# Optimization experiments

Hardware: AMD Instinct MI355X
Metric: run time of the kernel (lower is better)

## Reference

```python
import jax, jax.numpy as jnp
import numpy as np
from jax import lax

USER_NUM = 60000
ITEM_NUM = 40000
N_NODES = USER_NUM + ITEM_NUM
EMB = 64
NNZ = 3200000
N_LAYERS = 3
ALPHA = 0.1


def setup_inputs() -> dict:
    key = jax.random.key(0)
    k1, k2, k3, k4, k5 = jax.random.split(key, 5)
    rows = jax.random.randint(k1, (NNZ,), 0, N_NODES, dtype=jnp.int32)
    cols = jax.random.randint(k2, (NNZ,), 0, N_NODES, dtype=jnp.int32)
    # normalized adjacency values are small positives
    vals = jax.random.uniform(k3, (NNZ,), dtype=jnp.float32) * 0.05
    user_emb = jax.random.normal(k4, (USER_NUM, EMB), dtype=jnp.float32) * 0.1
    item_emb = jax.random.normal(k5, (ITEM_NUM, EMB), dtype=jnp.float32) * 0.1
    return {"rows": rows, "cols": cols, "vals": vals,
            "user_emb": user_emb, "item_emb": item_emb}


def reference(rows, cols, vals, user_emb, item_emb):
    # ego = cat(user, item); e_out starts at zeros (first forward call).
    ego = jnp.concatenate([user_emb, item_emb], axis=0)  # [N, d]
    e0 = jnp.zeros_like(ego)

    def step(e, _):
        # torch.sparse.mm(A, e.clone().detach()) -> SpMM with stop_gradient,
        # matching the original's detach of the propagated state.
        gathered = vals[:, None] * lax.stop_gradient(e)[cols]  # [nnz, d]
        msg = jax.ops.segment_sum(gathered, rows, num_segments=N_NODES)
        e_new = (1.0 - ALPHA) * msg + ego
        return e_new, None

    e_out, _ = lax.scan(step, e0, None, length=N_LAYERS)
    return e_out[:USER_NUM], e_out[USER_NUM:]
```

## Files before the change

kernel.cpp:

```cpp
#include <hip/hip_runtime.h>
#include <hip/hip_fp16.h>


#define USER_NUM 60000
#define ITEM_NUM 40000
#define N_NODES  100000
#define EMB      64
#define NNZ      3200000
#define OMA      0.9f
#define BR       128
#define NB       782
#define TILE     4096
#define CAPB     4480

typedef float f32x4 __attribute__((ext_vector_type(4)));

__global__ __launch_bounds__(256) void conv_init(const float* __restrict__ ue,
                                                 const float* __restrict__ ie,
                                                 __half* __restrict__ dst,
                                                 int* __restrict__ bcursor) {
    int t = blockIdx.x * 256 + threadIdx.x;
    if (t < NB) bcursor[t] = t * CAPB;
    const int total8 = N_NODES * EMB / 8;
    if (t >= total8) return;
    size_t f0 = (size_t)t * 8;
    const size_t usz = (size_t)USER_NUM * EMB;
    const float4* s4 = (f0 < usz) ? (const float4*)(ue + f0)
                                  : (const float4*)(ie + (f0 - usz));
    float4 x = s4[0], y = s4[1];
    union { float4 f4; __half2 h2[4]; } o;
    o.h2[0] = __floats2half2_rn(x.x, x.y);
    o.h2[1] = __floats2half2_rn(x.z, x.w);
    o.h2[2] = __floats2half2_rn(y.x, y.y);
    o.h2[3] = __floats2half2_rn(y.z, y.w);
    ((float4*)dst)[t] = o.f4;
}

__global__ __launch_bounds__(256) void bucket_scatter(const int* __restrict__ rows,
                                                      const int* __restrict__ cols,
                                                      const float* __restrict__ vals,
                                                      int* __restrict__ bcursor,
                                                      int2* __restrict__ ebuf) {
    __shared__ int bins[NB + 1];
    __shared__ int lcur[NB];
    __shared__ int wsum[4];
    __shared__ int2 stage[TILE];
    int t = threadIdx.x;
    int lane = t & 63, w = t >> 6;
    for (int b = t; b <= NB; b += 256) bins[b] = 0;
    __syncthreads();

    int e0 = blockIdx.x * TILE;
    int mybk[16], mypk[16];
    float myv[16];
#pragma unroll
    for (int j = 0; j < 16; ++j) {
        int i = e0 + t + 256 * j;
        mybk[j] = -1;
        if (i < NNZ) {
            int r = rows[i], c = cols[i];
            myv[j]  = vals[i] * OMA;
            mybk[j] = r >> 7;
            mypk[j] = c | ((r & 127) << 17);
            atomicAdd(&bins[mybk[j]], 1);
        }
    }
    __syncthreads();

    int b0 = t * 4;
    int r0 = (b0     < NB) ? bins[b0]     : 0;
    int r1 = (b0 + 1 < NB) ? bins[b0 + 1] : 0;
    int r2 = (b0 + 2 < NB) ? bins[b0 + 2] : 0;
    int r3 = (b0 + 3 < NB) ? bins[b0 + 3] : 0;
    int s = r0 + r1 + r2 + r3;
    int incl = s;
#pragma unroll
    for (int off = 1; off < 64; off <<= 1) {
        int v = __shfl_up(incl, off, 64);
        if (lane >= off) incl += v;
    }
    if (lane == 63) wsum[w] = incl;
    __syncthreads();
    int prefix = 0;
#pragma unroll
    for (int i = 0; i < 4; ++i) if (i < w) prefix += wsum[i];
    int excl = prefix + incl - s;
    if (b0     < NB) { bins[b0]     = excl; lcur[b0]     = excl; excl += r0; }
    if (b0 + 1 < NB) { bins[b0 + 1] = excl; lcur[b0 + 1] = excl; excl += r1; }
    if (b0 + 2 < NB) { bins[b0 + 2] = excl; lcur[b0 + 2] = excl; excl += r2; }
    if (b0 + 3 < NB) { bins[b0 + 3] = excl; lcur[b0 + 3] = excl; excl += r3; }
    if (t == 255) bins[NB] = prefix + incl;
    __syncthreads();

#pragma unroll
    for (int j = 0; j < 16; ++j) {
        if (mybk[j] >= 0) {
            int p = atomicAdd(&lcur[mybk[j]], 1);
            stage[p] = make_int2(mypk[j], __float_as_int(myv[j]));
        }
    }
    __syncthreads();

    for (int b = t; b < NB; b += 256) {
        int st = bins[b], en = bins[b + 1];
        int cnt = en - st;
        if (cnt > 0) lcur[b] = atomicAdd(&bcursor[b], cnt) - st;
    }
    __syncthreads();

    int total = bins[NB];
    for (int i = t; i < total; i += 256) {
        int lo = 0, hi = NB;
        while (hi - lo > 1) {
            int mid = (lo + hi) >> 1;
            if (bins[mid] <= i) lo = mid; else hi = mid;
        }
        ebuf[(size_t)(lcur[lo] + i)] = stage[i];
    }
}

__global__ __launch_bounds__(256) void sort_spmm1(const int* __restrict__ bcursor,
                                                  int2* __restrict__ ebuf,
                                                  int* __restrict__ row_start,
                                                  int* __restrict__ row_end,
                                                  const __half* __restrict__ ego_h,
                                                  const float* __restrict__ ue,
                                                  const float* __restrict__ ie,
                                                  __half* __restrict__ e2h) {
    __shared__ int2 stage[CAPB];
    __shared__ int rhist[BR], rofs[BR], rcur[BR];
    int bk = blockIdx.x, t = threadIdx.x;
    int s = bk * CAPB;
    int cnt = min(bcursor[bk] - s, CAPB);

    if (t < BR) rhist[t] = 0;
    __syncthreads();
    for (int i = t; i < cnt; i += 256) {
        int2 v = ebuf[(size_t)(s + i)];
        stage[i] = v;
        atomicAdd(&rhist[(v.x >> 17) & 127], 1);
    }
    __syncthreads();
    if (t < 64) {
        int h0 = rhist[2 * t], h1 = rhist[2 * t + 1];
        int pair = h0 + h1;
        int incl = pair;
#pragma unroll
        for (int off = 1; off < 64; off <<= 1) {
            int v = __shfl_up(incl, off, 64);
            if (t >= off) incl += v;
        }
        int base = incl - pair;
        rofs[2 * t]     = base;      rcur[2 * t]     = base;
        rofs[2 * t + 1] = base + h0; rcur[2 * t + 1] = base + h0;
    }
    __syncthreads();
    if (t < BR) {
        int r = (bk << 7) + t;
        if (r < N_NODES) {
            row_start[r] = s + rofs[t];
            row_end[r]   = s + rofs[t] + rhist[t];
        }
    }
    for (int i = t; i < cnt; i += 256) {
        int2 v = stage[i];
        int p = atomicAdd(&rcur[(v.x >> 17) & 127], 1);
        ebuf[(size_t)(s + p)] = v;
    }
    __syncthreads();

    int lane  = t & 15;
    int qbase = (t & 63) & ~15;
    int g = t >> 4;
    const float2* srcv = (const float2*)ego_h;
#pragma unroll
    for (int rr = 0; rr < 8; ++rr) {
        int rl = (g << 3) | rr;
        int r  = (bk << 7) + rl;
        if (r >= N_NODES) break;
        const float* egop = (r < USER_NUM) ? (ue + (size_t)r * EMB)
                                           : (ie + (size_t)(r - USER_NUM) * EMB);
        float4 acc = ((const float4*)egop)[lane];
        int ss = s + rofs[rl];
        int ee = ss + rhist[rl];
        int2 cv = (ss + lane < ee) ? ebuf[(size_t)(ss + lane)] : make_int2(0, 0);
        for (int k = ss; k < ee; k += 16) {
            int idxn = k + 16 + lane;
            int2 nv = (idxn < ee) ? ebuf[(size_t)idxn] : make_int2(0, 0);
#pragma unroll
            for (int j = 0; j < 16; ++j) {
                int   cj = __shfl(cv.x, qbase + j, 64) & 0x1FFFF;
                float vj = __int_as_float(__shfl(cv.y, qbase + j, 64));
                union { float2 f2; __half2 h2[2]; } u;
                u.f2 = srcv[(size_t)cj * 16 + lane];
                float2 a = __half22float2(u.h2[0]);
                float2 b = __half22float2(u.h2[1]);
                acc.x += vj * a.x; acc.y += vj * a.y;
                acc.z += vj * b.x; acc.w += vj * b.y;
            }
            cv = nv;
        }
        union { float2 f2; __half2 h2[2]; } o;
        o.h2[0] = __floats2half2_rn(acc.x, acc.y);
        o.h2[1] = __floats2half2_rn(acc.z, acc.w);
        ((float2*)e2h)[(size_t)r * 16 + lane] = o.f2;
    }
}

__global__ __launch_bounds__(256) void spmm2(const int* __restrict__ row_start,
                                             const int* __restrict__ row_end,
                                             const int2* __restrict__ colval,
                                             const __half* __restrict__ src,
                                             const float* __restrict__ ue,
                                             const float* __restrict__ ie,
                                             float* __restrict__ outb) {
    int tid = blockIdx.x * 256 + threadIdx.x;
    int r = tid >> 4;
    if (r >= N_NODES) return;
    int lane  = threadIdx.x & 15;
    int qbase = (threadIdx.x & 63) & ~15;

    const float* egop = (r < USER_NUM) ? (ue + (size_t)r * EMB)
                                       : (ie + (size_t)(r - USER_NUM) * EMB);
    float4 acc = ((const float4*)egop)[lane];
    const float2* srcv = (const float2*)src;
    int s = row_start[r], e = row_end[r];

    int2 cv = (s + lane < e) ? colval[(size_t)(s + lane)] : make_int2(0, 0);
    for (int k = s; k < e; k += 16) {
        int idxn = k + 16 + lane;
        int2 nv = (idxn < e) ? colval[(size_t)idxn] : make_int2(0, 0);
#pragma unroll
        for (int j = 0; j < 16; ++j) {
            int   cj = __shfl(cv.x, qbase + j, 64) & 0x1FFFF;
            float vj = __int_as_float(__shfl(cv.y, qbase + j, 64));
            union { float2 f2; __half2 h2[2]; } u;
            u.f2 = srcv[(size_t)cj * 16 + lane];
            float2 a = __half22float2(u.h2[0]);
            float2 b = __half22float2(u.h2[1]);
            acc.x += vj * a.x; acc.y += vj * a.y;
            acc.z += vj * b.x; acc.w += vj * b.y;
        }
        cv = nv;
    }
    f32x4 av = { acc.x, acc.y, acc.z, acc.w };
    __builtin_nontemporal_store(av, &((f32x4*)outb)[(size_t)r * 16 + lane]);
}

extern "C" void kernel_launch(void* const* d_in, const int* in_sizes, int n_in,
                              void* d_out, int out_size, void* d_ws, size_t ws_size,
                              hipStream_t stream) {
    const int*   rows = (const int*)d_in[0];
    const int*   cols = (const int*)d_in[1];
    const float* vals = (const float*)d_in[2];
    const float* ue   = (const float*)d_in[3];
    const float* ie   = (const float*)d_in[4];
    float* out = (float*)d_out;

    char* ws = (char*)d_ws;
    __half* ego_h    = (__half*)ws;
    __half* e2h      = (__half*)(ws + 12800000);
    int2*   ebuf     = (int2*)(ws + 25600000);
    int*    row_s    = (int*)(ws + 53626880);
    int*    row_e    = (int*)(ws + 54026880);
    int*    bcursor  = (int*)(ws + 54426880);

    const int convBlocks = (N_NODES * EMB / 8 + 255) / 256;
    conv_init<<<convBlocks, 256, 0, stream>>>(ue, ie, ego_h, bcursor);

    const int tiles = (NNZ + TILE - 1) / TILE;
    bucket_scatter<<<tiles, 256, 0, stream>>>(rows, cols, vals, bcursor, ebuf);
    sort_spmm1<<<NB, 256, 0, stream>>>(bcursor, ebuf, row_s, row_e, ego_h, ue, ie, e2h);

    const int spmmBlocks = (N_NODES * 16 + 255) / 256;
    spmm2<<<spmmBlocks, 256, 0, stream>>>(row_s, row_e, ebuf, e2h, ue, ie, out);
}
```

Measured before the change: 284.0 us.

## Fuse fp16 conversion into bucket scatter and halve row-bucket size

Folds the fp32-to-fp16 embedding conversion into the edge-bucketing kernel, so each block converts a slice of embeddings before binning edges. The separate init launch goes away and bcursor is zeroed with a memset. Rows per bucket drop from 128 to 64, doubling the bucket count so sort_spmm1 runs twice as many blocks with smaller LDS staging, which should improve occupancy and load balance. In exchange the per-tile prefix scan now covers 7 bins per thread, and each bucket's capacity is tighter (2432 slots for about 2048 expected edges), so a heavily loaded bucket could overflow.

New measurement: 316.1 us. +11.3%, slower.

```diff
diff --git a/kernel.cpp b/kernel.cpp
--- a/kernel.cpp
+++ b/kernel.cpp
@@ -8,45 +8,47 @@
 #define EMB      64
 #define NNZ      3200000
 #define OMA      0.9f
-#define BR       128
-#define NB       782
+#define BR       64
+#define NB       1563
 #define TILE     4096
-#define CAPB     4480
+#define CAPB     2432
 
 typedef float f32x4 __attribute__((ext_vector_type(4)));
 
-__global__ __launch_bounds__(256) void conv_init(const float* __restrict__ ue,
-                                                 const float* __restrict__ ie,
-                                                 __half* __restrict__ dst,
-                                                 int* __restrict__ bcursor) {
-    int t = blockIdx.x * 256 + threadIdx.x;
-    if (t < NB) bcursor[t] = t * CAPB;
-    const int total8 = N_NODES * EMB / 8;
-    if (t >= total8) return;
-    size_t f0 = (size_t)t * 8;
-    const size_t usz = (size_t)USER_NUM * EMB;
-    const float4* s4 = (f0 < usz) ? (const float4*)(ue + f0)
-                                  : (const float4*)(ie + (f0 - usz));
-    float4 x = s4[0], y = s4[1];
-    union { float4 f4; __half2 h2[4]; } o;
-    o.h2[0] = __floats2half2_rn(x.x, x.y);
-    o.h2[1] = __floats2half2_rn(x.z, x.w);
-    o.h2[2] = __floats2half2_rn(y.x, y.y);
-    o.h2[3] = __floats2half2_rn(y.z, y.w);
-    ((float4*)dst)[t] = o.f4;
-}
-
-__global__ __launch_bounds__(256) void bucket_scatter(const int* __restrict__ rows,
-                                                      const int* __restrict__ cols,
-                                                      const float* __restrict__ vals,
-                                                      int* __restrict__ bcursor,
-                                                      int2* __restrict__ ebuf) {
+__global__ __launch_bounds__(256) void conv_scatter(const int* __restrict__ rows,
+                                                    const int* __restrict__ cols,
+                                                    const float* __restrict__ vals,
+                                                    const float* __restrict__ ue,
+                                                    const float* __restrict__ ie,
+                                                    __half* __restrict__ ego_h,
+                                                    int* __restrict__ bcursor,
+                                                    int2* __restrict__ ebuf) {
     __shared__ int bins[NB + 1];
     __shared__ int lcur[NB];
     __shared__ int wsum[4];
     __shared__ int2 stage[TILE];
     int t = threadIdx.x;
     int lane = t & 63, w = t >> 6;
+
+    int gtid = blockIdx.x * 256 + t;
+    const size_t usz = (size_t)USER_NUM * EMB;
+#pragma unroll
+    for (int q = 0; q < 4; ++q) {
+        int it = gtid * 4 + q;
+        if (it < N_NODES * EMB / 8) {
+            size_t f0 = (size_t)it * 8;
+            const float4* s4 = (f0 < usz) ? (const float4*)(ue + f0)
+                                          : (const float4*)(ie + (f0 - usz));
+            float4 x = s4[0], y = s4[1];
+            union { float4 f4; __half2 h2[4]; } o;
+            o.h2[0] = __floats2half2_rn(x.x, x.y);
+            o.h2[1] = __floats2half2_rn(x.z, x.w);
+            o.h2[2] = __floats2half2_rn(y.x, y.y);
+            o.h2[3] = __floats2half2_rn(y.z, y.w);
+            ((float4*)ego_h)[it] = o.f4;
+        }
+    }
+
     for (int b = t; b <= NB; b += 256) bins[b] = 0;
     __syncthreads();
 
@@ -60,19 +62,21 @@
         if (i < NNZ) {
             int r = rows[i], c = cols[i];
             myv[j]  = vals[i] * OMA;
-            mybk[j] = r >> 7;
-            mypk[j] = c | ((r & 127) << 17);
+            mybk[j] = r >> 6;
+            mypk[j] = c | ((r & 63) << 17);
             atomicAdd(&bins[mybk[j]], 1);
         }
     }
     __syncthreads();
 
-    int b0 = t * 4;
-    int r0 = (b0     < NB) ? bins[b0]     : 0;
-    int r1 = (b0 + 1 < NB) ? bins[b0 + 1] : 0;
-    int r2 = (b0 + 2 < NB) ? bins[b0 + 2] : 0;
-    int r3 = (b0 + 3 < NB) ? bins[b0 + 3] : 0;
-    int s = r0 + r1 + r2 + r3;
+    int b0 = t * 7;
+    int rr[7];
+    int s = 0;
+#pragma unroll
+    for (int q = 0; q < 7; ++q) {
+        rr[q] = (b0 + q < NB) ? bins[b0 + q] : 0;
+        s += rr[q];
+    }
     int incl = s;
 #pragma unroll
     for (int off = 1; off < 64; off <<= 1) {
@@ -85,10 +89,11 @@
 #pragma unroll
     for (int i = 0; i < 4; ++i) if (i < w) prefix += wsum[i];
     int excl = prefix + incl - s;
-    if (b0     < NB) { bins[b0]     = excl; lcur[b0]     = excl; excl += r0; }
-    if (b0 + 1 < NB) { bins[b0 + 1] = excl; lcur[b0 + 1] = excl; excl += r1; }
-    if (b0 + 2 < NB) { bins[b0 + 2] = excl; lcur[b0 + 2] = excl; excl += r2; }
-    if (b0 + 3 < NB) { bins[b0 + 3] = excl; lcur[b0 + 3] = excl; excl += r3; }
+#pragma unroll
+    for (int q = 0; q < 7; ++q) {
+        int i = b0 + q;
+        if (i < NB) { bins[i] = excl; lcur[i] = excl; excl += rr[q]; }
+    }
     if (t == 255) bins[NB] = prefix + incl;
     __syncthreads();
 
@@ -104,7 +109,7 @@
     for (int b = t; b < NB; b += 256) {
         int st = bins[b], en = bins[b + 1];
         int cnt = en - st;
-        if (cnt > 0) lcur[b] = atomicAdd(&bcursor[b], cnt) - st;
+        if (cnt > 0) lcur[b] = b * CAPB + atomicAdd(&bcursor[b], cnt) - st;
     }
     __syncthreads();
 
@@ -131,40 +136,37 @@
     __shared__ int rhist[BR], rofs[BR], rcur[BR];
     int bk = blockIdx.x, t = threadIdx.x;
     int s = bk * CAPB;
-    int cnt = min(bcursor[bk] - s, CAPB);
+    int cnt = min(bcursor[bk], CAPB);
 
     if (t < BR) rhist[t] = 0;
     __syncthreads();
     for (int i = t; i < cnt; i += 256) {
         int2 v = ebuf[(size_t)(s + i)];
         stage[i] = v;
-        atomicAdd(&rhist[(v.x >> 17) & 127], 1);
+        atomicAdd(&rhist[(v.x >> 17) & 63], 1);
     }
     __syncthreads();
     if (t < 64) {
-        int h0 = rhist[2 * t], h1 = rhist[2 * t + 1];
-        int pair = h0 + h1;
-        int incl = pair;
+        int h = rhist[t];
+        int incl = h;
 #pragma unroll
         for (int off = 1; off < 64; off <<= 1) {
             int v = __shfl_up(incl, off, 64);
             if (t >= off) incl += v;
         }
-        int base = incl - pair;
-        rofs[2 * t]     = base;      rcur[2 * t]     = base;
-        rofs[2 * t + 1] = base + h0; rcur[2 * t + 1] = base + h0;
-    }
-    __syncthreads();
-    if (t < BR) {
-        int r = (bk << 7) + t;
+        int base = incl - h;
+        rofs[t] = base;
+        rcur[t] = base;
+        int r = (bk << 6) + t;
         if (r < N_NODES) {
-            row_start[r] = s + rofs[t];
-            row_end[r]   = s + rofs[t] + rhist[t];
-        }
-    }
+            row_start[r] = s + base;
+            row_end[r]   = s + base + h;
+        }
+    }
+    __syncthreads();
     for (int i = t; i < cnt; i += 256) {
         int2 v = stage[i];
-        int p = atomicAdd(&rcur[(v.x >> 17) & 127], 1);
+        int p = atomicAdd(&rcur[(v.x >> 17) & 63], 1);
         ebuf[(size_t)(s + p)] = v;
     }
     __syncthreads();
@@ -174,9 +176,9 @@
     int g = t >> 4;
     const float2* srcv = (const float2*)ego_h;
 #pragma unroll
-    for (int rr = 0; rr < 8; ++rr) {
-        int rl = (g << 3) | rr;
-        int r  = (bk << 7) + rl;
+    for (int q = 0; q < 4; ++q) {
+        int rl = (g << 2) | q;
+        int r  = (bk << 6) + rl;
         if (r >= N_NODES) break;
         const float* egop = (r < USER_NUM) ? (ue + (size_t)r * EMB)
                                            : (ie + (size_t)(r - USER_NUM) * EMB);
@@ -261,16 +263,17 @@
     __half* ego_h    = (__half*)ws;
     __half* e2h      = (__half*)(ws + 12800000);
     int2*   ebuf     = (int2*)(ws + 25600000);
-    int*    row_s    = (int*)(ws + 53626880);
-    int*    row_e    = (int*)(ws + 54026880);
-    int*    bcursor  = (int*)(ws + 54426880);
-
-    const int convBlocks = (N_NODES * EMB / 8 + 255) / 256;
-    conv_init<<<convBlocks, 256, 0, stream>>>(ue, ie, ego_h, bcursor);
+    int*    row_s    = (int*)(ws + 56009728);
+    int*    row_e    = (int*)(ws + 56409728);
+    int*    bcursor  = (int*)(ws + 56809728);
+
+    (void)hipMemsetAsync(bcursor, 0, NB * sizeof(int), stream);
 
     const int tiles = (NNZ + TILE - 1) / TILE;
-    bucket_scatter<<<tiles, 256, 0, stream>>>(rows, cols, vals, bcursor, ebuf);
-    sort_spmm1<<<NB, 256, 0, stream>>>(bcursor, ebuf, row_s, row_e, ego_h, ue, ie, e2h);
+    conv_scatter<<<tiles, 256, 0, stream>>>(rows, cols, vals, ue, ie,
+                                            ego_h, bcursor, ebuf);
+    sort_spmm1<<<NB, 256, 0, stream>>>(bcursor, ebuf, row_s, row_e,
+                                       ego_h, ue, ie, e2h);
 
     const int spmmBlocks = (N_NODES * 16 + 255) / 256;
     spmm2<<<spmmBlocks, 256, 0, stream>>>(row_s, row_e, ebuf, e2h, ue, ie, out);
```

## Fuse fp16 conversion into scatter and sub-sort row edges by column slice

Applied to the files above, without the earlier changes.

Folds the fp32-to-fp16 embedding conversion into the edge bucket-scatter kernel and replaces the cursor-init kernel with a memset, removing one launch. The per-bucket sort now keys on row plus a four-way column range, so each row's neighbours are gathered in column-slice order for better cache locality across rows. To fit the larger histogram in shared memory, edge values are staged as fp16, which slightly reduces the precision of the adjacency weights.

Result: slower. 304.4 us (+7.2%).

```diff
diff --git a/kernel.cpp b/kernel.cpp
--- a/kernel.cpp
+++ b/kernel.cpp
@@ -12,41 +12,44 @@
 #define NB       782
 #define TILE     4096
 #define CAPB     4480
+#define NKEY     512
 
 typedef float f32x4 __attribute__((ext_vector_type(4)));
 
-__global__ __launch_bounds__(256) void conv_init(const float* __restrict__ ue,
-                                                 const float* __restrict__ ie,
-                                                 __half* __restrict__ dst,
-                                                 int* __restrict__ bcursor) {
-    int t = blockIdx.x * 256 + threadIdx.x;
-    if (t < NB) bcursor[t] = t * CAPB;
-    const int total8 = N_NODES * EMB / 8;
-    if (t >= total8) return;
-    size_t f0 = (size_t)t * 8;
-    const size_t usz = (size_t)USER_NUM * EMB;
-    const float4* s4 = (f0 < usz) ? (const float4*)(ue + f0)
-                                  : (const float4*)(ie + (f0 - usz));
-    float4 x = s4[0], y = s4[1];
-    union { float4 f4; __half2 h2[4]; } o;
-    o.h2[0] = __floats2half2_rn(x.x, x.y);
-    o.h2[1] = __floats2half2_rn(x.z, x.w);
-    o.h2[2] = __floats2half2_rn(y.x, y.y);
-    o.h2[3] = __floats2half2_rn(y.z, y.w);
-    ((float4*)dst)[t] = o.f4;
-}
-
-__global__ __launch_bounds__(256) void bucket_scatter(const int* __restrict__ rows,
-                                                      const int* __restrict__ cols,
-                                                      const float* __restrict__ vals,
-                                                      int* __restrict__ bcursor,
-                                                      int2* __restrict__ ebuf) {
+__global__ __launch_bounds__(256) void conv_scatter(const int* __restrict__ rows,
+                                                    const int* __restrict__ cols,
+                                                    const float* __restrict__ vals,
+                                                    const float* __restrict__ ue,
+                                                    const float* __restrict__ ie,
+                                                    __half* __restrict__ ego_h,
+                                                    int* __restrict__ bcursor,
+                                                    int2* __restrict__ ebuf) {
     __shared__ int bins[NB + 1];
     __shared__ int lcur[NB];
     __shared__ int wsum[4];
     __shared__ int2 stage[TILE];
     int t = threadIdx.x;
     int lane = t & 63, w = t >> 6;
+
+    int gtid = blockIdx.x * 256 + t;
+    const size_t usz = (size_t)USER_NUM * EMB;
+#pragma unroll
+    for (int q = 0; q < 4; ++q) {
+        int it = gtid * 4 + q;
+        if (it < N_NODES * EMB / 8) {
+            size_t f0 = (size_t)it * 8;
+            const float4* s4 = (f0 < usz) ? (const float4*)(ue + f0)
+                                          : (const float4*)(ie + (f0 - usz));
+            float4 x = s4[0], y = s4[1];
+            union { float4 f4; __half2 h2[4]; } o;
+            o.h2[0] = __floats2half2_rn(x.x, x.y);
+            o.h2[1] = __floats2half2_rn(x.z, x.w);
+            o.h2[2] = __floats2half2_rn(y.x, y.y);
+            o.h2[3] = __floats2half2_rn(y.z, y.w);
+            ((float4*)ego_h)[it] = o.f4;
+        }
+    }
+
     for (int b = t; b <= NB; b += 256) bins[b] = 0;
     __syncthreads();
 
@@ -104,7 +107,7 @@
     for (int b = t; b < NB; b += 256) {
         int st = bins[b], en = bins[b + 1];
         int cnt = en - st;
-        if (cnt > 0) lcur[b] = atomicAdd(&bcursor[b], cnt) - st;
+        if (cnt > 0) lcur[b] = b * CAPB + atomicAdd(&bcursor[b], cnt) - st;
     }
     __syncthreads();
 
@@ -127,49 +130,68 @@
                                                   const float* __restrict__ ue,
                                                   const float* __restrict__ ie,
                                                   __half* __restrict__ e2h) {
-    __shared__ int2 stage[CAPB];
-    __shared__ int rhist[BR], rofs[BR], rcur[BR];
+    __shared__ int    pkbuf[CAPB];
+    __shared__ __half valbuf[CAPB];
+    __shared__ int rhist[NKEY], rofs[NKEY], rcur[NKEY];
+    __shared__ int wsum[4];
     int bk = blockIdx.x, t = threadIdx.x;
+    int lane = t & 63, w = t >> 6;
     int s = bk * CAPB;
-    int cnt = min(bcursor[bk] - s, CAPB);
-
-    if (t < BR) rhist[t] = 0;
+    int cnt = min(bcursor[bk], CAPB);
+
+    for (int b = t; b < NKEY; b += 256) rhist[b] = 0;
     __syncthreads();
     for (int i = t; i < cnt; i += 256) {
         int2 v = ebuf[(size_t)(s + i)];
-        stage[i] = v;
-        atomicAdd(&rhist[(v.x >> 17) & 127], 1);
-    }
-    __syncthreads();
-    if (t < 64) {
-        int h0 = rhist[2 * t], h1 = rhist[2 * t + 1];
-        int pair = h0 + h1;
-        int incl = pair;
-#pragma unroll
-        for (int off = 1; off < 64; off <<= 1) {
-            int v = __shfl_up(incl, off, 64);
-            if (t >= off) incl += v;
-        }
-        int base = incl - pair;
-        rofs[2 * t]     = base;      rcur[2 * t]     = base;
-        rofs[2 * t + 1] = base + h0; rcur[2 * t + 1] = base + h0;
-    }
-    __syncthreads();
+        pkbuf[i]  = v.x;
+        valbuf[i] = __float2half(__int_as_float(v.y));
+        int c  = v.x & 0x1FFFF;
+        int sl = (c >= 25000) + (c >= 50000) + (c >= 75000);
+        int key = (((v.x >> 17) & 127) << 2) | sl;
+        atomicAdd(&rhist[key], 1);
+    }
+    __syncthreads();
+
+    int b0 = t * 2;
+    int h0 = rhist[b0], h1 = rhist[b0 + 1];
+    int ss2 = h0 + h1;
+    int incl = ss2;
+#pragma unroll
+    for (int off = 1; off < 64; off <<= 1) {
+        int v = __shfl_up(incl, off, 64);
+        if (lane >= off) incl += v;
+    }
+    if (lane == 63) wsum[w] = incl;
+    __syncthreads();
+    int prefix = 0;
+#pragma unroll
+    for (int i = 0; i < 4; ++i) if (i < w) prefix += wsum[i];
+    int excl = prefix + incl - ss2;
+    rofs[b0] = excl;     rcur[b0] = excl;
+    rofs[b0 + 1] = excl + h0; rcur[b0 + 1] = excl + h0;
+    __syncthreads();
+
     if (t < BR) {
         int r = (bk << 7) + t;
         if (r < N_NODES) {
-            row_start[r] = s + rofs[t];
-            row_end[r]   = s + rofs[t] + rhist[t];
+            int st = rofs[t << 2];
+            int en = rofs[t << 2] + rhist[t << 2] + rhist[(t << 2) + 1]
+                   + rhist[(t << 2) + 2] + rhist[(t << 2) + 3];
+            row_start[r] = s + st;
+            row_end[r]   = s + en;
         }
     }
     for (int i = t; i < cnt; i += 256) {
-        int2 v = stage[i];
-        int p = atomicAdd(&rcur[(v.x >> 17) & 127], 1);
-        ebuf[(size_t)(s + p)] = v;
-    }
-    __syncthreads();
-
-    int lane  = t & 15;
+        int pk = pkbuf[i];
+        int c  = pk & 0x1FFFF;
+        int sl = (c >= 25000) + (c >= 50000) + (c >= 75000);
+        int key = (((pk >> 17) & 127) << 2) | sl;
+        int p = atomicAdd(&rcur[key], 1);
+        ebuf[(size_t)(s + p)] = make_int2(pk, __float_as_int(__half2float(valbuf[i])));
+    }
+    __syncthreads();
+
+    int l16   = t & 15;
     int qbase = (t & 63) & ~15;
     int g = t >> 4;
     const float2* srcv = (const float2*)ego_h;
@@ -180,19 +202,20 @@
         if (r >= N_NODES) break;
         const float* egop = (r < USER_NUM) ? (ue + (size_t)r * EMB)
                                            : (ie + (size_t)(r - USER_NUM) * EMB);
-        float4 acc = ((const float4*)egop)[lane];
-        int ss = s + rofs[rl];
-        int ee = ss + rhist[rl];
-        int2 cv = (ss + lane < ee) ? ebuf[(size_t)(ss + lane)] : make_int2(0, 0);
+        float4 acc = ((const float4*)egop)[l16];
+        int ss = s + rofs[rl << 2];
+        int ee = s + rofs[rl << 2] + rhist[rl << 2] + rhist[(rl << 2) + 1]
+               + rhist[(rl << 2) + 2] + rhist[(rl << 2) + 3];
+        int2 cv = (ss + l16 < ee) ? ebuf[(size_t)(ss + l16)] : make_int2(0, 0);
         for (int k = ss; k < ee; k += 16) {
-            int idxn = k + 16 + lane;
+            int idxn = k + 16 + l16;
             int2 nv = (idxn < ee) ? ebuf[(size_t)idxn] : make_int2(0, 0);
 #pragma unroll
             for (int j = 0; j < 16; ++j) {
                 int   cj = __shfl(cv.x, qbase + j, 64) & 0x1FFFF;
                 float vj = __int_as_float(__shfl(cv.y, qbase + j, 64));
                 union { float2 f2; __half2 h2[2]; } u;
-                u.f2 = srcv[(size_t)cj * 16 + lane];
+                u.f2 = srcv[(size_t)cj * 16 + l16];
                 float2 a = __half22float2(u.h2[0]);
                 float2 b = __half22float2(u.h2[1]);
                 acc.x += vj * a.x; acc.y += vj * a.y;
@@ -203,7 +226,7 @@
         union { float2 f2; __half2 h2[2]; } o;
         o.h2[0] = __floats2half2_rn(acc.x, acc.y);
         o.h2[1] = __floats2half2_rn(acc.z, acc.w);
-        ((float2*)e2h)[(size_t)r * 16 + lane] = o.f2;
+        ((float2*)e2h)[(size_t)r * 16 + l16] = o.f2;
     }
 }
 
@@ -265,12 +288,13 @@
     int*    row_e    = (int*)(ws + 54026880);
     int*    bcursor  = (int*)(ws + 54426880);
 
-    const int convBlocks = (N_NODES * EMB / 8 + 255) / 256;
-    conv_init<<<convBlocks, 256, 0, stream>>>(ue, ie, ego_h, bcursor);
+    (void)hipMemsetAsync(bcursor, 0, NB * sizeof(int), stream);
 
     const int tiles = (NNZ + TILE - 1) / TILE;
-    bucket_scatter<<<tiles, 256, 0, stream>>>(rows, cols, vals, bcursor, ebuf);
-    sort_spmm1<<<NB, 256, 0, stream>>>(bcursor, ebuf, row_s, row_e, ego_h, ue, ie, e2h);
+    conv_scatter<<<tiles, 256, 0, stream>>>(rows, cols, vals, ue, ie,
+                                            ego_h, bcursor, ebuf);
+    sort_spmm1<<<NB, 256, 0, stream>>>(bcursor, ebuf, row_s, row_e,
+                                       ego_h, ue, ie, e2h);
 
     const int spmmBlocks = (N_NODES * 16 + 255) / 256;
     spmm2<<<spmmBlocks, 256, 0, stream>>>(row_s, row_e, ebuf, e2h, ue, ie, out);
```
